# Kernel optimization log

Hardware: AMD Instinct MI355X
Metric: run time of the kernel (lower is better)

The kernel has to match this reference:

```python
import jax, jax.numpy as jnp
import numpy as np


def setup_inputs() -> dict:
    key = jax.random.key(0)
    k1, k2, k3 = jax.random.split(key, 3)
    B, T, F, H = 4, 2048, 256, 8
    x = jax.random.normal(k1, (B, T, F), dtype=jnp.float32)
    W_qkv = jax.random.normal(k2, (F, H * F * 3), dtype=jnp.float32) * (1.0 / np.sqrt(F))
    b_qkv = jnp.zeros((H * F * 3,), dtype=jnp.float32)
    W_proj = jax.random.normal(k3, (H * F, F), dtype=jnp.float32) * (1.0 / np.sqrt(H * F))
    b_proj = jnp.zeros((F,), dtype=jnp.float32)
    return {"x": x, "W_qkv": W_qkv, "b_qkv": b_qkv, "W_proj": W_proj, "b_proj": b_proj}


def reference(x, W_qkv, b_qkv, W_proj, b_proj):
    # x: [B, T, F]; heads H = 8, per-head dim = F (full in_features per head)
    B, T, F = x.shape
    H = W_qkv.shape[1] // (F * 3)
    temperature = 1.0
    qkv = x @ W_qkv + b_qkv                      # [B, T, H*F*3]
    qkv = qkv.reshape(B, T, H, F, 3)
    qkv = jnp.transpose(qkv, (0, 2, 1, 3, 4))    # [B, H, T, F, 3]
    inv_sqrt_f = 1.0 / jnp.sqrt(jnp.asarray(F, x.dtype))
    q = qkv[..., 0] * inv_sqrt_f                 # note: BOTH q and k scaled
    k = qkv[..., 1] * inv_sqrt_f
    v = qkv[..., 2]
    scores = jnp.einsum('bhtf,bhsf->bhts', q, k) / temperature  # [B, H, T, T]
    weights = jax.nn.softmax(scores, axis=-1)
    out = jnp.einsum('bhts,bhsf->bhtf', weights, v)              # [B, H, T, F]
    out = jnp.transpose(out, (0, 2, 1, 3)).reshape(B, T, H * F)  # [B, T, H*F]
    return out @ W_proj + b_proj                                 # [B, T, F]
```

## Files before the change

kernel.cpp:

```cpp
#include <hip/hip_runtime.h>
#include <hip/hip_bf16.h>


typedef __attribute__((ext_vector_type(8))) short bf16x8;
typedef __attribute__((ext_vector_type(4))) short s16x4;
typedef __attribute__((ext_vector_type(4))) float f32x4;
typedef __attribute__((ext_vector_type(16))) float f32x16;
typedef __attribute__((ext_vector_type(4))) int i32x4;

#define MFMA16(a, b, c) __builtin_amdgcn_mfma_f32_16x16x32_bf16((a), (b), (c), 0, 0, 0)
#define MFMA32(a, b, c) __builtin_amdgcn_mfma_f32_32x32x16_bf16((a), (b), (c), 0, 0, 0)

static __device__ __forceinline__ short bf16_bits(float v) {
    __hip_bfloat16 h = __float2bfloat16(v);
    return reinterpret_cast<short&>(h);
}

static __device__ __forceinline__ unsigned pack_bf16(float lo, float hi) {
    unsigned a = (unsigned)(unsigned short)bf16_bits(lo);
    unsigned b = (unsigned)(unsigned short)bf16_bits(hi);
    return a | (b << 16);
}

static __device__ __forceinline__ void dma_lds16(const void* g, void* l) {
    __builtin_amdgcn_global_load_lds((const __attribute__((address_space(1))) unsigned int*)g,
                                     (__attribute__((address_space(3))) unsigned int*)l,
                                     16, 0, 0);
}

static __device__ __forceinline__ i32x4 cvt8(const float* __restrict__ src) {
    f32x4 a = *(const f32x4*)(src);
    f32x4 b = *(const f32x4*)(src + 4);
    union { short s[8]; i32x4 v; } u;
#pragma unroll
    for (int i = 0; i < 4; ++i) {
        u.s[i]     = bf16_bits(a[i]);
        u.s[i + 4] = bf16_bits(b[i]);
    }
    return u.v;
}

__global__ __launch_bounds__(256) void k_cvt_x(const float* __restrict__ in,
                                               __hip_bfloat16* __restrict__ out) {
    size_t i = ((size_t)blockIdx.x * 256 + threadIdx.x) * 8;
    *(i32x4*)(out + i) = cvt8(in + i);
}

__global__ __launch_bounds__(256) void k_transpose_qkvw(const float* __restrict__ in,
                                                        __hip_bfloat16* __restrict__ out) {
    __shared__ __hip_bfloat16 tile[32][33];
    int tx = threadIdx.x & 31;
    int ty = threadIdx.x >> 5;
    int c0 = blockIdx.x * 32, r0 = blockIdx.y * 32;
#pragma unroll
    for (int j = 0; j < 4; ++j)
        tile[ty + j * 8][tx] = __float2bfloat16(in[(size_t)(r0 + ty + j * 8) * 6144 + c0 + tx]);
    __syncthreads();
#pragma unroll
    for (int j = 0; j < 4; ++j) {
        int n = c0 + ty + j * 8;
        int h = n / 768, rem = n - h * 768;
        int f = rem / 3, c = rem - f * 3;
        int np = c * 2048 + h * 256 + f;
        out[(size_t)np * 256 + r0 + tx] = tile[tx][ty + j * 8];
    }
}

__global__ __launch_bounds__(256) void k_transpose(const float* __restrict__ in,
                                                   __hip_bfloat16* __restrict__ out,
                                                   int rows, int cols) {
    __shared__ __hip_bfloat16 tile[32][33];
    int tx = threadIdx.x & 31;
    int ty = threadIdx.x >> 5;
    int c0 = blockIdx.x * 32, r0 = blockIdx.y * 32;
#pragma unroll
    for (int j = 0; j < 4; ++j)
        tile[ty + j * 8][tx] = __float2bfloat16(in[(size_t)(r0 + ty + j * 8) * cols + c0 + tx]);
    __syncthreads();
#pragma unroll
    for (int j = 0; j < 4; ++j)
        out[(size_t)(c0 + ty + j * 8) * rows + r0 + tx] = tile[tx][ty + j * 8];
}

#define GS 32
__global__ __launch_bounds__(256) void k_gemm_qkv(const __hip_bfloat16* __restrict__ X,
                                                  const __hip_bfloat16* __restrict__ Wt,
                                                  const float* __restrict__ bias,
                                                  __hip_bfloat16* __restrict__ Q,
                                                  __hip_bfloat16* __restrict__ K,
                                                  __hip_bfloat16* __restrict__ Vt) {
    __shared__ __align__(16) short As[128 * GS];
    __shared__ __align__(16) short Bs[128 * GS];
    const int tid = threadIdx.x;
    const int m0 = blockIdx.y * 128, n0 = blockIdx.x * 128;
    const int w = tid >> 6, lane = tid & 63, l16 = lane & 15, quad = lane >> 4;
    const int wm = (w >> 1) * 64, wn = (w & 1) * 64;

    f32x4 acc[4][4];
#pragma unroll
    for (int mi = 0; mi < 4; ++mi)
#pragma unroll
        for (int ni = 0; ni < 4; ++ni) acc[mi][ni] = (f32x4){0.f, 0.f, 0.f, 0.f};

    for (int k0 = 0; k0 < 256; k0 += 32) {
        __syncthreads();
#pragma unroll
        for (int p = 0; p < 2; ++p) {
            int ci = (w * 2 + p) * 64 + lane;
            int row = ci >> 2, col = (ci & 3) * 8;
            dma_lds16(X + (size_t)(m0 + row) * 256 + k0 + col, &As[(w * 2 + p) * 512]);
            dma_lds16(Wt + (size_t)(n0 + row) * 256 + k0 + col, &Bs[(w * 2 + p) * 512]);
        }
        __syncthreads();
        bf16x8 af[4], bfr[4];
#pragma unroll
        for (int mi = 0; mi < 4; ++mi)
            af[mi] = *(const bf16x8*)&As[(wm + mi * 16 + l16) * GS + quad * 8];
#pragma unroll
        for (int ni = 0; ni < 4; ++ni)
            bfr[ni] = *(const bf16x8*)&Bs[(wn + ni * 16 + l16) * GS + quad * 8];
#pragma unroll
        for (int mi = 0; mi < 4; ++mi)
#pragma unroll
            for (int ni = 0; ni < 4; ++ni)
                acc[mi][ni] = MFMA16(af[mi], bfr[ni], acc[mi][ni]);
    }

    const int c = n0 >> 11;
    if (c < 2) {
        __hip_bfloat16* dst = (c == 0) ? Q : K;
#pragma unroll
        for (int mi = 0; mi < 4; ++mi) {
#pragma unroll
            for (int ni = 0; ni < 4; ++ni) {
                int np = n0 + wn + ni * 16 + l16;
                int h = (np >> 8) & 7, f = np & 255;
                float bv = bias[h * 768 + f * 3 + c];
#pragma unroll
                for (int r = 0; r < 4; ++r) {
                    int m = m0 + wm + mi * 16 + quad * 4 + r;
                    int b = m >> 11, t = m & 2047;
                    dst[((size_t)(b * 8 + h) * 2048 + t) * 256 + f] =
                        __float2bfloat16((acc[mi][ni][r] + bv) * 0.0625f);
                }
            }
        }
    } else {
        const int pos = ((quad & 1) << 3) | ((quad >> 1) << 2);
#pragma unroll
        for (int mi = 0; mi < 4; ++mi) {
            int m = m0 + wm + mi * 16 + quad * 4;
            int b = m >> 11, t = m & 2047;
            size_t tcol = (size_t)(t & ~31) + ((mi & 1) << 4) + pos;
#pragma unroll
            for (int ni = 0; ni < 4; ++ni) {
                int np = n0 + wn + ni * 16 + l16;
                int h = (np >> 8) & 7, f = np & 255;
                float bv = bias[h * 768 + f * 3 + 2];
                s16x4 v;
#pragma unroll
                for (int r = 0; r < 4; ++r) v[r] = bf16_bits(acc[mi][ni][r] + bv);
                *(s16x4*)(Vt + ((size_t)(b * 8 + h) * 256 + f) * 2048 + tcol) = v;
            }
        }
    }
}

#define VSS 40
#define ES 40
__global__ __launch_bounds__(512) void k_flash(const __hip_bfloat16* __restrict__ Q,
                                               const __hip_bfloat16* __restrict__ K,
                                               const __hip_bfloat16* __restrict__ Vt,
                                               __hip_bfloat16* __restrict__ O) {
    __shared__ __align__(16) short Ks[2][32 * 256];
    __shared__ __align__(16) short Vs[2][256 * VSS];
    const int tid = threadIdx.x;
    const int w = tid >> 6, lane = tid & 63;
    const int l32 = lane & 31, hi = lane >> 5;
    const int bh = blockIdx.y;
    const int q0 = blockIdx.x * 256;
    const __hip_bfloat16* Qb = Q + (size_t)bh * 2048 * 256;
    const __hip_bfloat16* Kb = K + (size_t)bh * 2048 * 256;
    const __hip_bfloat16* Vb = Vt + (size_t)bh * 256 * 2048;

    bf16x8 qf[16];
    {
        const __hip_bfloat16* qrow_p = Qb + (size_t)(q0 + w * 32 + l32) * 256 + hi * 8;
#pragma unroll
        for (int kf = 0; kf < 16; ++kf) qf[kf] = *(const bf16x8*)(qrow_p + kf * 16);
    }

    f32x16 oacc[8];
#pragma unroll
    for (int nt = 0; nt < 8; ++nt)
#pragma unroll
        for (int r = 0; r < 16; ++r) oacc[nt][r] = 0.f;
    float lsum = 0.f;

    const int vrow = (tid >> 2);
    const int vcol = (tid & 3) * 8;

#pragma unroll
    for (int p = 0; p < 2; ++p) {
        int seg = w * 2 + p;
        int r = 2 * seg + hi;
        int clog = l32 ^ (r & 7);
        dma_lds16(Kb + (size_t)r * 256 + clog * 8, &Ks[0][seg * 512]);
    }
#pragma unroll
    for (int p = 0; p < 2; ++p) {
        int row = vrow + p * 128;
        *(i32x4*)&Vs[0][row * VSS + vcol] = *(const i32x4*)(Vb + (size_t)row * 2048 + vcol);
    }
    __syncthreads();

    const int s7 = l32 & 7;
    for (int it = 0; it < 64; ++it) {
        const int cur = it & 1, nxt = cur ^ 1;
        const bool more = it < 63;
        const int ktn = (it + 1) * 32;

        i32x4 vreg[2];
        if (more) {
#pragma unroll
            for (int p = 0; p < 2; ++p) {
                int seg = w * 2 + p;
                int r = 2 * seg + hi;
                int clog = l32 ^ (r & 7);
                dma_lds16(Kb + (size_t)(ktn + r) * 256 + clog * 8, &Ks[nxt][seg * 512]);
            }
#pragma unroll
            for (int p = 0; p < 2; ++p) {
                int row = vrow + p * 128;
                vreg[p] = *(const i32x4*)(Vb + (size_t)row * 2048 + ktn + vcol);
            }
        }

        f32x16 s;
#pragma unroll
        for (int r = 0; r < 16; ++r) s[r] = 0.f;
        const short* ksb = &Ks[cur][l32 * 256];
#pragma unroll
        for (int kf = 0; kf < 16; ++kf) {
            int g = kf * 2 + hi;
            bf16x8 kfr = *(const bf16x8*)&ksb[((g ^ s7) * 8)];
            s = MFMA32(kfr, qf[kf], s);
        }

#pragma unroll
        for (int kk = 0; kk < 2; ++kk) {
            unsigned ch[4];
#pragma unroll
            for (int c = 0; c < 4; ++c) {
                float e0 = __expf(s[8 * kk + 2 * c]);
                float e1 = __expf(s[8 * kk + 2 * c + 1]);
                lsum += e0 + e1;
                ch[c] = pack_bf16(e0, e1);
            }
            union { i32x4 i; bf16x8 v; } pf;
            pf.i = (i32x4){(int)ch[0], (int)ch[1], (int)ch[2], (int)ch[3]};

#pragma unroll
            for (int nt = 0; nt < 8; ++nt) {
                bf16x8 vf = *(const bf16x8*)&Vs[cur][(nt * 32 + l32) * VSS + kk * 16 + hi * 8];
                oacc[nt] = MFMA32(vf, pf.v, oacc[nt]);
            }
        }

        if (more) {
#pragma unroll
            for (int p = 0; p < 2; ++p) {
                int row = vrow + p * 128;
                *(i32x4*)&Vs[nxt][row * VSS + vcol] = vreg[p];
            }
        }
        __syncthreads();
    }

    lsum += __shfl_xor(lsum, 32);
    const float inv = 1.f / lsum;

    short* ebuf = &Ks[0][0] + w * (32 * ES);
    const int b = bh >> 3, hh = bh & 7;
#pragma unroll
    for (int nt = 0; nt < 8; ++nt) {
#pragma unroll
        for (int r = 0; r < 16; ++r) {
            int fl = (r & 3) + 8 * (r >> 2) + 4 * hi;
            ebuf[l32 * ES + fl] = bf16_bits(oacc[nt][r] * inv);
        }
        asm volatile("s_waitcnt lgkmcnt(0)" ::: "memory");
#pragma unroll
        for (int p = 0; p < 2; ++p) {
            i32x4 v = *(const i32x4*)&ebuf[(lane >> 1) * ES + (lane & 1) * 8 + p * 16];
            int t = q0 + w * 32 + (lane >> 1);
            __hip_bfloat16* dst =
                O + ((size_t)(b * 2048 + t) * 2048 + hh * 256 + nt * 32 + (lane & 1) * 8 + p * 16);
            *(i32x4*)dst = v;
        }
        asm volatile("s_waitcnt lgkmcnt(0)" ::: "memory");
    }
}

__global__ __launch_bounds__(256) void k_gemm_proj(const __hip_bfloat16* __restrict__ A,
                                                   const __hip_bfloat16* __restrict__ Wt,
                                                   const float* __restrict__ bias,
                                                   float* __restrict__ Out) {
    __shared__ __align__(16) short As[128 * GS];
    __shared__ __align__(16) short Bs[64 * GS];
    const int tid = threadIdx.x;
    const int m0 = blockIdx.y * 128, n0 = blockIdx.x * 64;
    const int w = tid >> 6, lane = tid & 63, l16 = lane & 15, quad = lane >> 4;
    const int wm = w * 32;

    f32x4 acc[2][4];
#pragma unroll
    for (int mi = 0; mi < 2; ++mi)
#pragma unroll
        for (int ni = 0; ni < 4; ++ni) acc[mi][ni] = (f32x4){0.f, 0.f, 0.f, 0.f};

    for (int k0 = 0; k0 < 2048; k0 += 32) {
        __syncthreads();
#pragma unroll
        for (int p = 0; p < 2; ++p) {
            int ci = (w * 2 + p) * 64 + lane;
            int row = ci >> 2, col = (ci & 3) * 8;
            dma_lds16(A + (size_t)(m0 + row) * 2048 + k0 + col, &As[(w * 2 + p) * 512]);
        }
        {
            int ci = w * 64 + lane;
            int row = ci >> 2, col = (ci & 3) * 8;
            dma_lds16(Wt + (size_t)(n0 + row) * 2048 + k0 + col, &Bs[w * 512]);
        }
        __syncthreads();
        bf16x8 af[2], bfr[4];
#pragma unroll
        for (int mi = 0; mi < 2; ++mi)
            af[mi] = *(const bf16x8*)&As[(wm + mi * 16 + l16) * GS + quad * 8];
#pragma unroll
        for (int ni = 0; ni < 4; ++ni)
            bfr[ni] = *(const bf16x8*)&Bs[(ni * 16 + l16) * GS + quad * 8];
#pragma unroll
        for (int mi = 0; mi < 2; ++mi)
#pragma unroll
            for (int ni = 0; ni < 4; ++ni)
                acc[mi][ni] = MFMA16(af[mi], bfr[ni], acc[mi][ni]);
    }

#pragma unroll
    for (int mi = 0; mi < 2; ++mi)
#pragma unroll
        for (int ni = 0; ni < 4; ++ni) {
            int n = n0 + ni * 16 + l16;
            float bv = bias[n];
#pragma unroll
            for (int r = 0; r < 4; ++r) {
                int m = m0 + wm + mi * 16 + quad * 4 + r;
                Out[(size_t)m * 256 + n] = acc[mi][ni][r] + bv;
            }
        }
}

extern "C" void kernel_launch(void* const* d_in, const int* in_sizes, int n_in,
                              void* d_out, int out_size, void* d_ws, size_t ws_size,
                              hipStream_t stream) {
    const float* x      = (const float*)d_in[0];
    const float* W_qkv  = (const float*)d_in[1];
    const float* b_qkv  = (const float*)d_in[2];
    const float* W_proj = (const float*)d_in[3];
    const float* b_proj = (const float*)d_in[4];
    float* out = (float*)d_out;

    const size_t E = 32ull * 2048 * 256;
    __hip_bfloat16* Qb     = (__hip_bfloat16*)d_ws;
    __hip_bfloat16* Kb     = Qb + E;
    __hip_bfloat16* Vt     = Kb + E;
    __hip_bfloat16* attn   = Vt + E;
    __hip_bfloat16* WqkvT  = attn + E;
    __hip_bfloat16* WprojT = WqkvT + 6144 * 256;
    __hip_bfloat16* Xb     = attn;

    k_cvt_x<<<dim3(8192 * 256 / (256 * 8)), 256, 0, stream>>>(x, Xb);
    k_transpose_qkvw<<<dim3(6144 / 32, 256 / 32), 256, 0, stream>>>(W_qkv, WqkvT);
    k_transpose<<<dim3(256 / 32, 2048 / 32), 256, 0, stream>>>(W_proj, WprojT, 2048, 256);
    k_gemm_qkv<<<dim3(48, 64), 256, 0, stream>>>(Xb, WqkvT, b_qkv, Qb, Kb, Vt);
    k_flash<<<dim3(8, 32), 512, 0, stream>>>(Qb, Kb, Vt, attn);
    k_gemm_proj<<<dim3(4, 64), 256, 0, stream>>>(attn, WprojT, b_proj, out);
}
```

Baseline: 300.2 us.

## Shrink flash blocks to 256 threads, DMA V tiles into swizzled LDS, remap grid

The attention kernel now runs 256-thread blocks handling 128 query rows, launched as a 1D grid of 512 blocks with a remapped head/query order and two blocks per CU. V tiles move from register-staged global loads with a padded stride to direct global-to-LDS DMA into an unpadded, XOR-swizzled layout, and the MFMA loops are wrapped in s_setprio hints. The aim is more resident blocks, fewer registers and fewer LDS write instructions, with better overlap between waves. In exchange each block reloads the full K/V stream for half as many queries, doubling K/V traffic.

After: 303.2 us. Within noise of the previous version (+1.0%).

```diff
diff --git a/kernel.cpp b/kernel.cpp
--- a/kernel.cpp
+++ b/kernel.cpp
@@ -166,19 +166,22 @@
     }
 }
 
-#define VSS 40
 #define ES 40
-__global__ __launch_bounds__(512) void k_flash(const __hip_bfloat16* __restrict__ Q,
-                                               const __hip_bfloat16* __restrict__ K,
-                                               const __hip_bfloat16* __restrict__ Vt,
-                                               __hip_bfloat16* __restrict__ O) {
+__global__ __launch_bounds__(256, 2) void k_flash(const __hip_bfloat16* __restrict__ Q,
+                                                  const __hip_bfloat16* __restrict__ K,
+                                                  const __hip_bfloat16* __restrict__ Vt,
+                                                  __hip_bfloat16* __restrict__ O) {
     __shared__ __align__(16) short Ks[2][32 * 256];
-    __shared__ __align__(16) short Vs[2][256 * VSS];
+    __shared__ __align__(16) short Vs[2][256 * 32];
     const int tid = threadIdx.x;
     const int w = tid >> 6, lane = tid & 63;
     const int l32 = lane & 31, hi = lane >> 5;
-    const int bh = blockIdx.y;
-    const int q0 = blockIdx.x * 256;
+
+    const int id = blockIdx.x;
+    const int slot = id >> 3;
+    const int bh = (id & 7) * 4 + (slot & 3);
+    const int q0 = (slot >> 2) * 128;
+
     const __hip_bfloat16* Qb = Q + (size_t)bh * 2048 * 256;
     const __hip_bfloat16* Kb = K + (size_t)bh * 2048 * 256;
     const __hip_bfloat16* Vb = Vt + (size_t)bh * 256 * 2048;
@@ -197,42 +200,43 @@
         for (int r = 0; r < 16; ++r) oacc[nt][r] = 0.f;
     float lsum = 0.f;
 
-    const int vrow = (tid >> 2);
-    const int vcol = (tid & 3) * 8;
-
-#pragma unroll
-    for (int p = 0; p < 2; ++p) {
-        int seg = w * 2 + p;
+    const int vrow = tid >> 2;
+    const int vchunk = (tid & 3) ^ (vrow & 3);
+
+#pragma unroll
+    for (int p = 0; p < 4; ++p) {
+        int seg = w * 4 + p;
         int r = 2 * seg + hi;
         int clog = l32 ^ (r & 7);
         dma_lds16(Kb + (size_t)r * 256 + clog * 8, &Ks[0][seg * 512]);
     }
 #pragma unroll
-    for (int p = 0; p < 2; ++p) {
-        int row = vrow + p * 128;
-        *(i32x4*)&Vs[0][row * VSS + vcol] = *(const i32x4*)(Vb + (size_t)row * 2048 + vcol);
+    for (int p = 0; p < 4; ++p) {
+        int row = vrow + p * 64;
+        dma_lds16(Vb + (size_t)row * 2048 + vchunk * 8, &Vs[0][(p * 64 + w * 16) * 32]);
     }
     __syncthreads();
 
     const int s7 = l32 & 7;
+    const int vx = l32 & 3;
     for (int it = 0; it < 64; ++it) {
         const int cur = it & 1, nxt = cur ^ 1;
         const bool more = it < 63;
         const int ktn = (it + 1) * 32;
 
-        i32x4 vreg[2];
         if (more) {
 #pragma unroll
-            for (int p = 0; p < 2; ++p) {
-                int seg = w * 2 + p;
+            for (int p = 0; p < 4; ++p) {
+                int seg = w * 4 + p;
                 int r = 2 * seg + hi;
                 int clog = l32 ^ (r & 7);
                 dma_lds16(Kb + (size_t)(ktn + r) * 256 + clog * 8, &Ks[nxt][seg * 512]);
             }
 #pragma unroll
-            for (int p = 0; p < 2; ++p) {
-                int row = vrow + p * 128;
-                vreg[p] = *(const i32x4*)(Vb + (size_t)row * 2048 + ktn + vcol);
+            for (int p = 0; p < 4; ++p) {
+                int row = vrow + p * 64;
+                dma_lds16(Vb + (size_t)row * 2048 + ktn + vchunk * 8,
+                          &Vs[nxt][(p * 64 + w * 16) * 32]);
             }
         }
 
@@ -240,12 +244,14 @@
 #pragma unroll
         for (int r = 0; r < 16; ++r) s[r] = 0.f;
         const short* ksb = &Ks[cur][l32 * 256];
+        __builtin_amdgcn_s_setprio(1);
 #pragma unroll
         for (int kf = 0; kf < 16; ++kf) {
             int g = kf * 2 + hi;
             bf16x8 kfr = *(const bf16x8*)&ksb[((g ^ s7) * 8)];
             s = MFMA32(kfr, qf[kf], s);
         }
+        __builtin_amdgcn_s_setprio(0);
 
 #pragma unroll
         for (int kk = 0; kk < 2; ++kk) {
@@ -260,20 +266,16 @@
             union { i32x4 i; bf16x8 v; } pf;
             pf.i = (i32x4){(int)ch[0], (int)ch[1], (int)ch[2], (int)ch[3]};
 
+            __builtin_amdgcn_s_setprio(1);
 #pragma unroll
             for (int nt = 0; nt < 8; ++nt) {
-                bf16x8 vf = *(const bf16x8*)&Vs[cur][(nt * 32 + l32) * VSS + kk * 16 + hi * 8];
+                bf16x8 vf = *(const bf16x8*)
+                    &Vs[cur][(nt * 32 + l32) * 32 + (((kk * 2 + hi) ^ vx) * 8)];
                 oacc[nt] = MFMA32(vf, pf.v, oacc[nt]);
             }
-        }
-
-        if (more) {
-#pragma unroll
-            for (int p = 0; p < 2; ++p) {
-                int row = vrow + p * 128;
-                *(i32x4*)&Vs[nxt][row * VSS + vcol] = vreg[p];
-            }
-        }
+            __builtin_amdgcn_s_setprio(0);
+        }
+
         __syncthreads();
     }
 
@@ -384,6 +386,6 @@
     k_transpose_qkvw<<<dim3(6144 / 32, 256 / 32), 256, 0, stream>>>(W_qkv, WqkvT);
     k_transpose<<<dim3(256 / 32, 2048 / 32), 256, 0, stream>>>(W_proj, WprojT, 2048, 256);
     k_gemm_qkv<<<dim3(48, 64), 256, 0, stream>>>(Xb, WqkvT, b_qkv, Qb, Kb, Vt);
-    k_flash<<<dim3(8, 32), 512, 0, stream>>>(Qb, Kb, Vt, attn);
+    k_flash<<<dim3(512), 256, 0, stream>>>(Qb, Kb, Vt, attn);
     k_gemm_proj<<<dim3(4, 64), 256, 0, stream>>>(attn, WprojT, b_proj, out);
 }
```

## Double-buffer LDS loads in both GEMMs and remap flash block-to-head order

Applied to the files above, without the earlier changes.

Both GEMM kernels now use two LDS buffers and issue the global-to-LDS DMA for the next K-slice before computing the current one. Explicit vmcnt waits and raw barriers replace the two __syncthreads per iteration, so memory latency can overlap MFMA work. The flash kernel switches to a 1D grid with a remapped block index that spreads consecutive blocks across heads, likely to balance K/V traffic across XCDs and L2. Double buffering doubles LDS use per block and relies on the hand-counted vmcnt values being correct.

After: 294.2 us. 1.02x faster.

```diff
diff --git a/kernel.cpp b/kernel.cpp
--- a/kernel.cpp
+++ b/kernel.cpp
@@ -89,41 +89,57 @@
                                                   __hip_bfloat16* __restrict__ Q,
                                                   __hip_bfloat16* __restrict__ K,
                                                   __hip_bfloat16* __restrict__ Vt) {
-    __shared__ __align__(16) short As[128 * GS];
-    __shared__ __align__(16) short Bs[128 * GS];
+    __shared__ __align__(16) short As[2][128 * GS];
+    __shared__ __align__(16) short Bs[2][128 * GS];
     const int tid = threadIdx.x;
     const int m0 = blockIdx.y * 128, n0 = blockIdx.x * 128;
     const int w = tid >> 6, lane = tid & 63, l16 = lane & 15, quad = lane >> 4;
     const int wm = (w >> 1) * 64, wn = (w & 1) * 64;
 
+    const int ci0 = (w * 2 + 0) * 64 + lane, ci1 = (w * 2 + 1) * 64 + lane;
+    const int r0s = ci0 >> 2, c0s = (ci0 & 3) * 8;
+    const int r1s = ci1 >> 2, c1s = (ci1 & 3) * 8;
+
     f32x4 acc[4][4];
 #pragma unroll
     for (int mi = 0; mi < 4; ++mi)
 #pragma unroll
         for (int ni = 0; ni < 4; ++ni) acc[mi][ni] = (f32x4){0.f, 0.f, 0.f, 0.f};
 
-    for (int k0 = 0; k0 < 256; k0 += 32) {
-        __syncthreads();
-#pragma unroll
-        for (int p = 0; p < 2; ++p) {
-            int ci = (w * 2 + p) * 64 + lane;
-            int row = ci >> 2, col = (ci & 3) * 8;
-            dma_lds16(X + (size_t)(m0 + row) * 256 + k0 + col, &As[(w * 2 + p) * 512]);
-            dma_lds16(Wt + (size_t)(n0 + row) * 256 + k0 + col, &Bs[(w * 2 + p) * 512]);
-        }
-        __syncthreads();
+    dma_lds16(X + (size_t)(m0 + r0s) * 256 + c0s, &As[0][(w * 2 + 0) * 512]);
+    dma_lds16(Wt + (size_t)(n0 + r0s) * 256 + c0s, &Bs[0][(w * 2 + 0) * 512]);
+    dma_lds16(X + (size_t)(m0 + r1s) * 256 + c1s, &As[0][(w * 2 + 1) * 512]);
+    dma_lds16(Wt + (size_t)(n0 + r1s) * 256 + c1s, &Bs[0][(w * 2 + 1) * 512]);
+
+    for (int it = 0; it < 8; ++it) {
+        const int cur = it & 1, nxt = cur ^ 1;
+        if (it < 7) {
+            const int k0 = (it + 1) * 32;
+            dma_lds16(X + (size_t)(m0 + r0s) * 256 + k0 + c0s, &As[nxt][(w * 2 + 0) * 512]);
+            dma_lds16(Wt + (size_t)(n0 + r0s) * 256 + k0 + c0s, &Bs[nxt][(w * 2 + 0) * 512]);
+            dma_lds16(X + (size_t)(m0 + r1s) * 256 + k0 + c1s, &As[nxt][(w * 2 + 1) * 512]);
+            dma_lds16(Wt + (size_t)(n0 + r1s) * 256 + k0 + c1s, &Bs[nxt][(w * 2 + 1) * 512]);
+            asm volatile("s_waitcnt vmcnt(4)" ::: "memory");
+        } else {
+            asm volatile("s_waitcnt vmcnt(0)" ::: "memory");
+        }
+        __builtin_amdgcn_s_barrier();
+
         bf16x8 af[4], bfr[4];
 #pragma unroll
         for (int mi = 0; mi < 4; ++mi)
-            af[mi] = *(const bf16x8*)&As[(wm + mi * 16 + l16) * GS + quad * 8];
+            af[mi] = *(const bf16x8*)&As[cur][(wm + mi * 16 + l16) * GS + quad * 8];
 #pragma unroll
         for (int ni = 0; ni < 4; ++ni)
-            bfr[ni] = *(const bf16x8*)&Bs[(wn + ni * 16 + l16) * GS + quad * 8];
+            bfr[ni] = *(const bf16x8*)&Bs[cur][(wn + ni * 16 + l16) * GS + quad * 8];
 #pragma unroll
         for (int mi = 0; mi < 4; ++mi)
 #pragma unroll
             for (int ni = 0; ni < 4; ++ni)
                 acc[mi][ni] = MFMA16(af[mi], bfr[ni], acc[mi][ni]);
+
+        asm volatile("s_waitcnt lgkmcnt(0)" ::: "memory");
+        __builtin_amdgcn_s_barrier();
     }
 
     const int c = n0 >> 11;
@@ -177,8 +193,12 @@
     const int tid = threadIdx.x;
     const int w = tid >> 6, lane = tid & 63;
     const int l32 = lane & 31, hi = lane >> 5;
-    const int bh = blockIdx.y;
-    const int q0 = blockIdx.x * 256;
+
+    const int id = blockIdx.x;
+    const int slot = id >> 3;
+    const int bh = (id & 7) * 4 + (slot & 3);
+    const int q0 = (slot >> 2) * 256;
+
     const __hip_bfloat16* Qb = Q + (size_t)bh * 2048 * 256;
     const __hip_bfloat16* Kb = K + (size_t)bh * 2048 * 256;
     const __hip_bfloat16* Vb = Vt + (size_t)bh * 256 * 2048;
@@ -306,45 +326,57 @@
                                                    const __hip_bfloat16* __restrict__ Wt,
                                                    const float* __restrict__ bias,
                                                    float* __restrict__ Out) {
-    __shared__ __align__(16) short As[128 * GS];
-    __shared__ __align__(16) short Bs[64 * GS];
+    __shared__ __align__(16) short As[2][128 * GS];
+    __shared__ __align__(16) short Bs[2][64 * GS];
     const int tid = threadIdx.x;
     const int m0 = blockIdx.y * 128, n0 = blockIdx.x * 64;
     const int w = tid >> 6, lane = tid & 63, l16 = lane & 15, quad = lane >> 4;
     const int wm = w * 32;
 
+    const int ciA0 = (w * 2 + 0) * 64 + lane, ciA1 = (w * 2 + 1) * 64 + lane;
+    const int rA0 = ciA0 >> 2, cA0 = (ciA0 & 3) * 8;
+    const int rA1 = ciA1 >> 2, cA1 = (ciA1 & 3) * 8;
+    const int ciB = w * 64 + lane;
+    const int rB = ciB >> 2, cB = (ciB & 3) * 8;
+
     f32x4 acc[2][4];
 #pragma unroll
     for (int mi = 0; mi < 2; ++mi)
 #pragma unroll
         for (int ni = 0; ni < 4; ++ni) acc[mi][ni] = (f32x4){0.f, 0.f, 0.f, 0.f};
 
-    for (int k0 = 0; k0 < 2048; k0 += 32) {
-        __syncthreads();
-#pragma unroll
-        for (int p = 0; p < 2; ++p) {
-            int ci = (w * 2 + p) * 64 + lane;
-            int row = ci >> 2, col = (ci & 3) * 8;
-            dma_lds16(A + (size_t)(m0 + row) * 2048 + k0 + col, &As[(w * 2 + p) * 512]);
-        }
-        {
-            int ci = w * 64 + lane;
-            int row = ci >> 2, col = (ci & 3) * 8;
-            dma_lds16(Wt + (size_t)(n0 + row) * 2048 + k0 + col, &Bs[w * 512]);
-        }
-        __syncthreads();
+    dma_lds16(A + (size_t)(m0 + rA0) * 2048 + cA0, &As[0][(w * 2 + 0) * 512]);
+    dma_lds16(A + (size_t)(m0 + rA1) * 2048 + cA1, &As[0][(w * 2 + 1) * 512]);
+    dma_lds16(Wt + (size_t)(n0 + rB) * 2048 + cB, &Bs[0][w * 512]);
+
+    for (int it = 0; it < 64; ++it) {
+        const int cur = it & 1, nxt = cur ^ 1;
+        if (it < 63) {
+            const int k0 = (it + 1) * 32;
+            dma_lds16(A + (size_t)(m0 + rA0) * 2048 + k0 + cA0, &As[nxt][(w * 2 + 0) * 512]);
+            dma_lds16(A + (size_t)(m0 + rA1) * 2048 + k0 + cA1, &As[nxt][(w * 2 + 1) * 512]);
+            dma_lds16(Wt + (size_t)(n0 + rB) * 2048 + k0 + cB, &Bs[nxt][w * 512]);
+            asm volatile("s_waitcnt vmcnt(3)" ::: "memory");
+        } else {
+            asm volatile("s_waitcnt vmcnt(0)" ::: "memory");
+        }
+        __builtin_amdgcn_s_barrier();
+
         bf16x8 af[2], bfr[4];
 #pragma unroll
         for (int mi = 0; mi < 2; ++mi)
-            af[mi] = *(const bf16x8*)&As[(wm + mi * 16 + l16) * GS + quad * 8];
+            af[mi] = *(const bf16x8*)&As[cur][(wm + mi * 16 + l16) * GS + quad * 8];
 #pragma unroll
         for (int ni = 0; ni < 4; ++ni)
-            bfr[ni] = *(const bf16x8*)&Bs[(ni * 16 + l16) * GS + quad * 8];
+            bfr[ni] = *(const bf16x8*)&Bs[cur][(ni * 16 + l16) * GS + quad * 8];
 #pragma unroll
         for (int mi = 0; mi < 2; ++mi)
 #pragma unroll
             for (int ni = 0; ni < 4; ++ni)
                 acc[mi][ni] = MFMA16(af[mi], bfr[ni], acc[mi][ni]);
+
+        asm volatile("s_waitcnt lgkmcnt(0)" ::: "memory");
+        __builtin_amdgcn_s_barrier();
     }
 
 #pragma unroll
@@ -384,6 +416,6 @@
     k_transpose_qkvw<<<dim3(6144 / 32, 256 / 32), 256, 0, stream>>>(W_qkv, WqkvT);
     k_transpose<<<dim3(256 / 32, 2048 / 32), 256, 0, stream>>>(W_proj, WprojT, 2048, 256);
     k_gemm_qkv<<<dim3(48, 64), 256, 0, stream>>>(Xb, WqkvT, b_qkv, Qb, Kb, Vt);
-    k_flash<<<dim3(8, 32), 512, 0, stream>>>(Qb, Kb, Vt, attn);
+    k_flash<<<dim3(256), 512, 0, stream>>>(Qb, Kb, Vt, attn);
     k_gemm_proj<<<dim3(4, 64), 256, 0, stream>>>(attn, WprojT, b_proj, out);
 }
```
